# Performance work log

Hardware: AMD Instinct MI355X
Metric: run time of the kernel (lower is better)

## Reference

```python
import jax, jax.numpy as jnp
import numpy as np

B, S_EN, S_FR, EMB, UNITS, V_EN, V_FR = 64, 64, 64, 512, 1024, 32000, 16000


def setup_inputs() -> dict:
    key = jax.random.key(0)
    ks = jax.random.split(key, 16)
    sc = 0.05
    inp = {
        "en": jax.random.randint(ks[0], (B, S_EN), 0, V_EN, dtype=jnp.int32),
        "fr": jax.random.randint(ks[1], (B, S_FR), 0, V_FR, dtype=jnp.int32),
        "valid_len": jax.random.randint(ks[2], (B,), 1, S_EN, dtype=jnp.int32),
        "en_emb": jax.random.normal(ks[3], (V_EN, EMB), jnp.float32) * sc,
        "de_emb": jax.random.normal(ks[4], (V_FR, EMB), jnp.float32) * sc,
        "en_W": jax.random.normal(ks[5], (EMB, 4 * UNITS), jnp.float32) * sc,
        "en_U": jax.random.normal(ks[6], (UNITS, 4 * UNITS), jnp.float32) * sc,
        "en_b": jnp.zeros((4 * UNITS,), jnp.float32),
        "de_W": jax.random.normal(ks[7], (UNITS + EMB, 4 * UNITS), jnp.float32) * sc,
        "de_U": jax.random.normal(ks[8], (UNITS, 4 * UNITS), jnp.float32) * sc,
        "de_b": jnp.zeros((4 * UNITS,), jnp.float32),
        "Wq": jax.random.normal(ks[9], (UNITS, UNITS), jnp.float32) * sc,
        "Wk": jax.random.normal(ks[10], (UNITS, UNITS), jnp.float32) * sc,
        "wv": jax.random.normal(ks[11], (UNITS, 1), jnp.float32) * sc,
        "Wd": jax.random.normal(ks[12], (UNITS, V_FR), jnp.float32) * sc,
        "bd": jnp.zeros((V_FR,), jnp.float32),
    }
    return inp


def _lstm_step(h, c, x, W, Uw, b):
    # keras gate order: i, f, g(candidate), o
    z = x @ W + h @ Uw + b
    i, f, g, o = jnp.split(z, 4, axis=-1)
    c = jax.nn.sigmoid(f) * c + jax.nn.sigmoid(i) * jnp.tanh(g)
    h = jax.nn.sigmoid(o) * jnp.tanh(c)
    return h, c


def reference(en, fr, valid_len, en_emb, de_emb, en_W, en_U, en_b,
              de_W, de_U, de_b, Wq, Wk, wv, Wd, bd):
    b = en.shape[0]
    u = en_U.shape[0]
    # ----- Encode -----
    x_en = en_emb[en]                       # (B, S_en, E)
    h0 = jnp.zeros((b, u), x_en.dtype)

    def enc_step(carry, xt):
        h, c = carry
        h, c = _lstm_step(h, c, xt, en_W, en_U, en_b)
        return (h, c), h

    (h, c), en_o = jax.lax.scan(enc_step, (h0, h0), jnp.swapaxes(x_en, 0, 1))
    en_o = jnp.swapaxes(en_o, 0, 1)         # (B, S_en, U)

    # ----- Decode with additive attention per step -----
    kproj = en_o @ Wk                       # (B, S_en, U), key proj is step-invariant
    pos = jnp.arange(en.shape[1])
    attn_mask = pos[None, :] < valid_len[:, None]   # (B, S_en)
    x_fr = de_emb[fr]                       # (B, S_fr, E)

    def dec_step(carry, xt):
        h, c = carry
        q = h @ Wq                          # (B, U)
        feat = jnp.tanh(q[:, None, :] + kproj)      # (B, S_en, U)
        score = jnp.squeeze(feat @ wv, -1)          # (B, S_en)
        score = jnp.where(attn_mask, score, -1000000.0)
        attn = jax.nn.softmax(score, axis=-1)
        context = jnp.einsum('bs,bsu->bu', attn, en_o)
        x = jnp.concatenate([context, xt], axis=-1)  # (B, U+E)
        h, c = _lstm_step(h, c, x, de_W, de_U, de_b)
        return (h, c), h

    (_, _), hs = jax.lax.scan(dec_step, (h, c), jnp.swapaxes(x_fr, 0, 1))
    logits = jnp.swapaxes(hs, 0, 1) @ Wd + bd       # (B, S_fr, V_fr)
    return logits
```

## Files before the change

### kernel.cpp

```cpp
#include <hip/hip_runtime.h>
#include <math.h>

#define BD    64
#define SEQ   64
#define EMBD  512
#define UNITS 1024
#define NG    4096
#define VFR   16000

typedef __attribute__((ext_vector_type(8))) short bf16x8;
typedef __attribute__((ext_vector_type(4))) float f32x4;

__device__ __forceinline__ float sigm(float x) { return 1.0f / (1.0f + __expf(-x)); }
__device__ __forceinline__ float tanh_f(float x) {
    float e = __expf(2.0f * x);
    return 1.0f - 2.0f / (e + 1.0f);
}
__device__ __forceinline__ unsigned bf16bits(float v) {
    unsigned u = __float_as_uint(v);
    return (u + 0x7FFFu + ((u >> 16) & 1u)) >> 16;
}
__device__ __forceinline__ float bf2f(short s) {
    return __uint_as_float(((unsigned)(unsigned short)s) << 16);
}
__device__ __forceinline__ void split2(float v, short& h, short& l) {
    unsigned hb = bf16bits(v);
    float hv = __uint_as_float(hb << 16);
    h = (short)hb;
    l = (short)bf16bits(v - hv);
}

__device__ __forceinline__ void gbar(int* cnt, int* gen, int nb) {
    __threadfence();
    __syncthreads();
    if (threadIdx.x == 0) {
        int g = __hip_atomic_load(gen, __ATOMIC_RELAXED, __HIP_MEMORY_SCOPE_AGENT);
        if (atomicAdd(cnt, 1) == nb - 1) {
            __hip_atomic_store(cnt, 0, __ATOMIC_RELAXED, __HIP_MEMORY_SCOPE_AGENT);
            __hip_atomic_store(gen, g + 1, __ATOMIC_RELEASE, __HIP_MEMORY_SCOPE_AGENT);
        } else {
            while (__hip_atomic_load(gen, __ATOMIC_RELAXED, __HIP_MEMORY_SCOPE_AGENT) == g)
                __builtin_amdgcn_s_sleep(8);
        }
    }
    __syncthreads();
    __threadfence();
}

__global__ __launch_bounds__(64) void zero16(int* p) {
    if (threadIdx.x < 16) p[threadIdx.x] = 0;
}

__global__ __launch_bounds__(256) void gather_bf16(
    const float* __restrict__ emb, const int* __restrict__ idx,
    short* __restrict__ dst, int K)
{
    int row = blockIdx.x;
    int g = idx[row];
    const float* src = emb + (size_t)g * K;
    for (int k = threadIdx.x * 2; k < K; k += 512) {
        float2 v = *(const float2*)&src[k];
        dst[(size_t)row * K + k]     = (short)bf16bits(v.x);
        dst[(size_t)row * K + k + 1] = (short)bf16bits(v.y);
    }
}

template <bool SPLIT>
__global__ __launch_bounds__(256) void transp_split(
    const float* __restrict__ src, int N, int K,
    short* __restrict__ dh, short* __restrict__ dl)
{
    __shared__ float sm[32][33];
    const int tid = threadIdx.x;
    const int nt = blockIdx.x * 32, kt = blockIdx.y * 32;
    {
        int r = tid >> 3, c4 = (tid & 7) * 4;
        float4 v = *(const float4*)&src[(size_t)(kt + r) * N + nt + c4];
        sm[r][c4] = v.x; sm[r][c4 + 1] = v.y; sm[r][c4 + 2] = v.z; sm[r][c4 + 3] = v.w;
    }
    __syncthreads();
    {
        int n = tid >> 3, k4 = (tid & 7) * 4;
        short4 hh, ll;
        short a, b;
        split2(sm[k4 + 0][n], a, b); hh.x = a; ll.x = b;
        split2(sm[k4 + 1][n], a, b); hh.y = a; ll.y = b;
        split2(sm[k4 + 2][n], a, b); hh.z = a; ll.z = b;
        split2(sm[k4 + 3][n], a, b); hh.w = a; ll.w = b;
        *(short4*)&dh[(size_t)(nt + n) * K + kt + k4] = hh;
        if (SPLIT) *(short4*)&dl[(size_t)(nt + n) * K + kt + k4] = ll;
    }
}

template <int OMODE, bool SA, bool SB>
__global__ __launch_bounds__(256, 2) void gemm_split(
    const short* __restrict__ Ah, const short* __restrict__ Al,
    const short* __restrict__ Bh, const short* __restrict__ Bl,
    const float* __restrict__ bias, void* __restrict__ Cout, int N, int K)
{
    __shared__ short lds[32 * 512];
    const int tid = threadIdx.x;
    const int lane = tid & 63, w = tid >> 6;
    const int bm = blockIdx.y, bn = blockIdx.x;
    const int wm = w & 1, wn = w >> 1;
    const int r15 = lane & 15, q = lane >> 4;

    f32x4 zero4 = {0.f, 0.f, 0.f, 0.f};
    f32x4 acc[4][4];
#pragma unroll
    for (int i = 0; i < 4; ++i)
#pragma unroll
        for (int j = 0; j < 4; ++j) acc[i][j] = zero4;

    const short* gsrc[8];
    bool use[8];
#pragma unroll
    for (int i = 0; i < 8; ++i) {
        int st = w * 8 + i;
        int mat = st >> 4, hl = (st >> 3) & 1, mt = st & 7;
        const short* base = (mat == 0) ? (hl ? Al : Ah) : (hl ? Bl : Bh);
        use[i] = (mat == 0) ? (SA || hl == 0) : (SB || hl == 0);
        int row = ((mat == 0) ? bm : bn) * 128 + mt * 16 + r15;
        gsrc[i] = base + (size_t)row * K + q * 8;
    }

    for (int k0 = 0; k0 < K; k0 += 32) {
        int4 stg[8];
#pragma unroll
        for (int i = 0; i < 8; ++i)
            if (use[i]) stg[i] = *(const int4*)(gsrc[i] + k0);
        __syncthreads();
#pragma unroll
        for (int i = 0; i < 8; ++i)
            if (use[i]) *(int4*)&lds[(size_t)((w * 8 + i) * 64 + lane) * 8] = stg[i];
        __syncthreads();

        bf16x8 ah[4], al[4], bh[4], bl[4];
#pragma unroll
        for (int i = 0; i < 4; ++i) {
            ah[i] = *(const bf16x8*)&lds[(((wm * 4 + i) * 64) + lane) * 8];
            if (SA) al[i] = *(const bf16x8*)&lds[(((8 + wm * 4 + i) * 64) + lane) * 8];
            bh[i] = *(const bf16x8*)&lds[(((16 + wn * 4 + i) * 64) + lane) * 8];
            if (SB) bl[i] = *(const bf16x8*)&lds[(((24 + wn * 4 + i) * 64) + lane) * 8];
        }
#pragma unroll
        for (int i = 0; i < 4; ++i)
#pragma unroll
            for (int j = 0; j < 4; ++j) {
                acc[i][j] = __builtin_amdgcn_mfma_f32_16x16x32_bf16(ah[i], bh[j], acc[i][j], 0, 0, 0);
                if (SA) acc[i][j] = __builtin_amdgcn_mfma_f32_16x16x32_bf16(al[i], bh[j], acc[i][j], 0, 0, 0);
                if (SB) acc[i][j] = __builtin_amdgcn_mfma_f32_16x16x32_bf16(ah[i], bl[j], acc[i][j], 0, 0, 0);
            }
    }

#pragma unroll
    for (int i = 0; i < 4; ++i) {
        int rowbase = bm * 128 + wm * 64 + i * 16 + q * 4;
#pragma unroll
        for (int j = 0; j < 4; ++j) {
            int col = bn * 128 + wn * 64 + j * 16 + r15;
            float bv = bias ? bias[col] : 0.f;
#pragma unroll
            for (int rI = 0; rI < 4; ++rI) {
                int row = rowbase + rI;
                float v = acc[i][j][rI] + bv;
                if (OMODE == 1) {
                    int orow = ((row & 63) << 6) | (row >> 6);
                    ((float*)Cout)[(size_t)orow * N + col] = v;
                } else if (OMODE == 0) {
                    ((float*)Cout)[(size_t)row * N + col] = v;
                } else {
                    ((short*)Cout)[(size_t)row * N + col] = (short)bf16bits(v);
                }
            }
        }
    }
}

__device__ __forceinline__ void accum_hU(
    float& a0, float& a1, const float* __restrict__ h_ws,
    const float* __restrict__ U, int n, int b0, int tid,
    float (*hsm)[66])
{
    for (int k0 = 0; k0 < 1024; k0 += 64) {
        __syncthreads();
#pragma unroll
        for (int i = 0; i < 2; ++i) {
            int idx4 = tid * 2 + i;
            int bb = idx4 >> 4, kq = (idx4 & 15) * 4;
            float4 v = *(const float4*)&h_ws[bb * 1024 + k0 + kq];
            hsm[kq + 0][bb] = v.x;
            hsm[kq + 1][bb] = v.y;
            hsm[kq + 2][bb] = v.z;
            hsm[kq + 3][bb] = v.w;
        }
        __syncthreads();
#pragma unroll 8
        for (int kk = 0; kk < 64; ++kk) {
            float uv = U[(size_t)(k0 + kk) * NG + n];
            float2 hv = *(const float2*)&hsm[kk][b0];
            a0 += hv.x * uv;
            a1 += hv.y * uv;
        }
    }
}

__device__ __forceinline__ void lstm_gate_phase(
    int t, int blk, int tid, const float* __restrict__ z_ws,
    float* __restrict__ h_ws, float* __restrict__ c_ws,
    short* __restrict__ oh, short* __restrict__ ol)
{
    int g2 = blk * 512 + tid;
    if (g2 < 65536) {
        int b = g2 >> 10, u = g2 & 1023;
        const float* zr = z_ws + b * NG;
        float zi = zr[u], zf = zr[u + 1024], zg = zr[u + 2048], zo = zr[u + 3072];
        float cp = c_ws[g2];
        float cn = sigm(zf) * cp + sigm(zi) * tanh_f(zg);
        float hn = sigm(zo) * tanh_f(cn);
        c_ws[g2] = cn;
        h_ws[g2] = hn;
        short hh, hl;
        split2(hn, hh, hl);
        size_t o = (size_t)(t * 64 + b) * 1024 + u;
        oh[o] = hh;
        ol[o] = hl;
    }
}

__global__ __launch_bounds__(512, 2) void encoder_persist(
    const short* __restrict__ xW,
    const float* __restrict__ U,
    float* __restrict__ h_ws, float* __restrict__ c_ws, float* __restrict__ z_ws,
    short* __restrict__ eo_h, short* __restrict__ eo_l,
    int* cnt, int* gen)
{
    __shared__ float hsm[64][66];
    const int tid = threadIdx.x;
    const int blk = blockIdx.x;
    {
        int g = blk * 512 + tid;
        if (g < 65536) h_ws[g] = 0.f;
        else c_ws[g - 65536] = 0.f;
    }
    gbar(cnt, gen, 256);
    const int c16 = tid & 15, bg = tid >> 4;
    const int n = blk * 16 + c16;
    const int b0 = bg * 2;
    for (int t = 0; t < SEQ; ++t) {
        float a0 = bf2f(xW[(size_t)(b0 * 64 + t) * NG + n]);
        float a1 = bf2f(xW[(size_t)((b0 + 1) * 64 + t) * NG + n]);
        accum_hU(a0, a1, h_ws, U, n, b0, tid, hsm);
        z_ws[b0 * NG + n] = a0;
        z_ws[(b0 + 1) * NG + n] = a1;
        gbar(cnt, gen, 256);
        lstm_gate_phase(t, blk, tid, z_ws, h_ws, c_ws, eo_h, eo_l);
        gbar(cnt, gen, 256);
    }
}

__global__ __launch_bounds__(512, 2) void decoder_persist(
    const short* __restrict__ xW,
    const float* __restrict__ U,
    const float* __restrict__ Wq, const float* __restrict__ wv,
    const float* __restrict__ kproj,
    const float* __restrict__ EOWc,
    const int* __restrict__ valid_len,
    float* __restrict__ h_ws, float* __restrict__ c_ws, float* __restrict__ z_ws,
    float* __restrict__ q_ws, float* __restrict__ sc_ws,
    short* __restrict__ hs_h, short* __restrict__ hs_l,
    int* cnt, int* gen)
{
    __shared__ float hsm[64][66];
    __shared__ float attn_sm[64][65];
    __shared__ float redq[64][8][4];
    const int tid = threadIdx.x;
    const int blk = blockIdx.x;

    for (int t = 0; t < SEQ; ++t) {
        {
            const int b = tid & 63;
            const int p8 = tid >> 6;
            const int kbase = p8 * 128;
            const int u0 = blk * 4;
            float ax = 0.f, ay = 0.f, az = 0.f, aw = 0.f;
            const float* hrow = h_ws + b * 1024 + kbase;
            const float* wbase = Wq + (size_t)kbase * 1024 + u0;
#pragma unroll 8
            for (int k = 0; k < 128; k += 4) {
                float4 hv = *(const float4*)&hrow[k];
                float4 w0 = *(const float4*)&wbase[(size_t)(k + 0) * 1024];
                float4 w1 = *(const float4*)&wbase[(size_t)(k + 1) * 1024];
                float4 w2 = *(const float4*)&wbase[(size_t)(k + 2) * 1024];
                float4 w3 = *(const float4*)&wbase[(size_t)(k + 3) * 1024];
                ax += hv.x * w0.x + hv.y * w1.x + hv.z * w2.x + hv.w * w3.x;
                ay += hv.x * w0.y + hv.y * w1.y + hv.z * w2.y + hv.w * w3.y;
                az += hv.x * w0.z + hv.y * w1.z + hv.z * w2.z + hv.w * w3.z;
                aw += hv.x * w0.w + hv.y * w1.w + hv.z * w2.w + hv.w * w3.w;
            }
            redq[b][p8][0] = ax; redq[b][p8][1] = ay;
            redq[b][p8][2] = az; redq[b][p8][3] = aw;
            __syncthreads();
            if (tid < 64) {
                float sx = 0.f, sy = 0.f, sz = 0.f, sw = 0.f;
#pragma unroll
                for (int p = 0; p < 8; ++p) {
                    sx += redq[tid][p][0]; sy += redq[tid][p][1];
                    sz += redq[tid][p][2]; sw += redq[tid][p][3];
                }
                float4 o = {sx, sy, sz, sw};
                *(float4*)&q_ws[tid * 1024 + u0] = o;
            }
        }
        gbar(cnt, gen, 256);
        {
            const int p = tid >> 5, l32 = tid & 31;
            const int pair = blk * 16 + p;
            const int b = pair & 63, s = pair >> 6;
            const float* kp = kproj + (size_t)pair * 1024;
            const float* qp = q_ws + b * 1024;
            float a = 0.f;
#pragma unroll
            for (int j = 0; j < 8; ++j) {
                int k = j * 128 + l32 * 4;
                float4 kv = *(const float4*)&kp[k];
                float4 qv = *(const float4*)&qp[k];
                float4 w4 = *(const float4*)&wv[k];
                a += w4.x * tanh_f(qv.x + kv.x);
                a += w4.y * tanh_f(qv.y + kv.y);
                a += w4.z * tanh_f(qv.z + kv.z);
                a += w4.w * tanh_f(qv.w + kv.w);
            }
#pragma unroll
            for (int off = 16; off; off >>= 1) a += __shfl_xor(a, off, 64);
            if (l32 == 0) sc_ws[b * 64 + s] = a;
        }
        gbar(cnt, gen, 256);
        {
            if (tid < 64) {
                const int b = tid;
                const int vl = valid_len[b];
                float mx = -1e30f;
                for (int s = 0; s < 64; ++s) {
                    float v = (s < vl) ? sc_ws[b * 64 + s] : -1000000.0f;
                    attn_sm[b][s] = v;
                    mx = fmaxf(mx, v);
                }
                float sum = 0.f;
                for (int s = 0; s < 64; ++s) {
                    float e = __expf(attn_sm[b][s] - mx);
                    attn_sm[b][s] = e;
                    sum += e;
                }
                float r = 1.f / sum;
                for (int s = 0; s < 64; ++s) attn_sm[b][s] *= r;
            }
            __syncthreads();
            const int c16 = tid & 15, bg = tid >> 4;
            const int n = blk * 16 + c16;
            const int b0 = bg * 2;
            float a0 = bf2f(xW[(size_t)(b0 * 64 + t) * NG + n]);
            float a1 = bf2f(xW[(size_t)((b0 + 1) * 64 + t) * NG + n]);
#pragma unroll 4
            for (int s = 0; s < 64; ++s) {
                float w0 = attn_sm[b0][s], w1 = attn_sm[b0 + 1][s];
                a0 += w0 * EOWc[(size_t)(s * 64 + b0) * NG + n];
                a1 += w1 * EOWc[(size_t)(s * 64 + b0 + 1) * NG + n];
            }
            accum_hU(a0, a1, h_ws, U, n, b0, tid, hsm);
            z_ws[b0 * NG + n] = a0;
            z_ws[(b0 + 1) * NG + n] = a1;
        }
        gbar(cnt, gen, 256);
        lstm_gate_phase(t, blk, tid, z_ws, h_ws, c_ws, hs_h, hs_l);
        gbar(cnt, gen, 256);
    }
}

extern "C" void kernel_launch(void* const* d_in, const int* in_sizes, int n_in,
                              void* d_out, int out_size, void* d_ws, size_t ws_size,
                              hipStream_t stream)
{
    const int*   en        = (const int*)d_in[0];
    const int*   fr        = (const int*)d_in[1];
    const int*   valid_len = (const int*)d_in[2];
    const float* en_emb    = (const float*)d_in[3];
    const float* de_emb    = (const float*)d_in[4];
    const float* en_W      = (const float*)d_in[5];
    const float* en_U      = (const float*)d_in[6];
    const float* en_b      = (const float*)d_in[7];
    const float* de_W      = (const float*)d_in[8];
    const float* de_U      = (const float*)d_in[9];
    const float* de_b      = (const float*)d_in[10];
    const float* Wq        = (const float*)d_in[11];
    const float* Wk        = (const float*)d_in[12];
    const float* wv        = (const float*)d_in[13];
    const float* Wd        = (const float*)d_in[14];
    const float* bd        = (const float*)d_in[15];
    float* out = (float*)d_out;
    char*  ws  = (char*)d_ws;

    float* EOWC  = (float*)(ws + 0);
    short* WDT_H = (short*)(ws + 0);
    short* WDT_L = (short*)(ws + 33554432);
    short* XWEN  = (short*)(ws + 67108864);
    float* KPROJ = (float*)(ws + 67108864);
    short* XWFR  = (short*)(ws + 100663296);
    short* XEN   = (short*)(ws + 134217728);
    short* XFR   = (short*)(ws + 138412032);
    short* WCT_H = (short*)(ws + 134217728);
    short* WCT_L = (short*)(ws + 142606336);
    short* HS_H  = (short*)(ws + 134217728);
    short* HS_L  = (short*)(ws + 142606336);
    short* ENWT  = (short*)(ws + 150994944);
    short* WXT   = (short*)(ws + 155189248);
    short* EO_H  = (short*)(ws + 150994944);
    short* EO_L  = (short*)(ws + 159383552);
    short* WKT_H = (short*)(ws + 167772160);
    short* WKT_L = (short*)(ws + 169869312);
    float* ZWS   = (float*)(ws + 171966464);
    float* HWS   = (float*)(ws + 173015040);
    float* CWS   = (float*)(ws + 173277184);
    float* QWS   = (float*)(ws + 173539328);
    float* SCWS  = (float*)(ws + 173801472);
    int*   BAR   = (int*)(ws + 173817856);

    zero16<<<1, 64, 0, stream>>>(BAR);

    gather_bf16<<<4096, 256, 0, stream>>>(en_emb, en, XEN, EMBD);
    gather_bf16<<<4096, 256, 0, stream>>>(de_emb, fr, XFR, EMBD);
    transp_split<false><<<dim3(128, 16), 256, 0, stream>>>(en_W, NG, EMBD, ENWT, nullptr);
    transp_split<false><<<dim3(128, 16), 256, 0, stream>>>(de_W + (size_t)UNITS * NG, NG, EMBD, WXT, nullptr);

    gemm_split<2, false, false><<<dim3(32, 32), 256, 0, stream>>>(
        XEN, XEN, ENWT, ENWT, en_b, XWEN, NG, EMBD);
    gemm_split<2, false, false><<<dim3(32, 32), 256, 0, stream>>>(
        XFR, XFR, WXT, WXT, de_b, XWFR, NG, EMBD);

    transp_split<true><<<dim3(128, 32), 256, 0, stream>>>(de_W, NG, UNITS, WCT_H, WCT_L);

    encoder_persist<<<256, 512, 0, stream>>>(XWEN, en_U, HWS, CWS, ZWS, EO_H, EO_L, BAR, BAR + 8);

    gemm_split<0, true, true><<<dim3(32, 32), 256, 0, stream>>>(
        EO_H, EO_L, WCT_H, WCT_L, nullptr, EOWC, NG, UNITS);

    transp_split<true><<<dim3(32, 32), 256, 0, stream>>>(Wk, UNITS, UNITS, WKT_H, WKT_L);
    gemm_split<0, true, true><<<dim3(8, 32), 256, 0, stream>>>(
        EO_H, EO_L, WKT_H, WKT_L, nullptr, KPROJ, UNITS, UNITS);

    decoder_persist<<<256, 512, 0, stream>>>(
        XWFR, de_U, Wq, wv, KPROJ, EOWC, valid_len,
        HWS, CWS, ZWS, QWS, SCWS, HS_H, HS_L, BAR, BAR + 8);

    transp_split<true><<<dim3(500, 32), 256, 0, stream>>>(Wd, VFR, UNITS, WDT_H, WDT_L);
    gemm_split<1, true, true><<<dim3(125, 32), 256, 0, stream>>>(
        HS_H, HS_L, WDT_H, WDT_L, bd, out, VFR, UNITS);
}
```

Before: 42.00 ms.

## Transpose recurrent weights and encoder-context product for contiguous vectorized loads

Adds an fp32 transpose kernel and pre-transposes the encoder and decoder recurrent weight matrices, so each thread reads its weight column as contiguous float4 vectors held in registers. The encoder-output times context-weight GEMM now writes in a layout where the sequence axis is innermost, so the decoder's attention-weighted context sum becomes contiguous float4 loads. The attention LDS row is padded to 68 floats to keep float4 reads aligned. This removes strided scalar global loads in the latency-bound recurrent loops, at the cost of extra transpose passes, more workspace, and higher register pressure.

```diff
diff --git a/kernel.cpp b/kernel.cpp
--- a/kernel.cpp
+++ b/kernel.cpp
@@ -92,6 +92,27 @@
     }
 }
 
+__global__ __launch_bounds__(256) void transp_f32(
+    const float* __restrict__ src, int N, int K, float* __restrict__ dst)
+{
+    __shared__ float sm[32][33];
+    const int tid = threadIdx.x;
+    const int nt = blockIdx.x * 32, kt = blockIdx.y * 32;
+    {
+        int r = tid >> 3, c4 = (tid & 7) * 4;
+        float4 v = *(const float4*)&src[(size_t)(kt + r) * N + nt + c4];
+        sm[r][c4] = v.x; sm[r][c4 + 1] = v.y; sm[r][c4 + 2] = v.z; sm[r][c4 + 3] = v.w;
+    }
+    __syncthreads();
+    {
+        int n = tid >> 3, k4 = (tid & 7) * 4;
+        float4 o;
+        o.x = sm[k4 + 0][n]; o.y = sm[k4 + 1][n];
+        o.z = sm[k4 + 2][n]; o.w = sm[k4 + 3][n];
+        *(float4*)&dst[(size_t)(nt + n) * K + kt + k4] = o;
+    }
+}
+
 template <int OMODE, bool SA, bool SB>
 __global__ __launch_bounds__(256, 2) void gemm_split(
     const short* __restrict__ Ah, const short* __restrict__ Al,
@@ -169,6 +190,8 @@
                     ((float*)Cout)[(size_t)orow * N + col] = v;
                 } else if (OMODE == 0) {
                     ((float*)Cout)[(size_t)row * N + col] = v;
+                } else if (OMODE == 3) {
+                    ((float*)Cout)[((size_t)(row & 63) * N + col) * 64 + (row >> 6)] = v;
                 } else {
                     ((short*)Cout)[(size_t)row * N + col] = (short)bf16bits(v);
                 }
@@ -177,12 +200,16 @@
     }
 }
 
-__device__ __forceinline__ void accum_hU(
+__device__ __forceinline__ void accum_hUT(
     float& a0, float& a1, const float* __restrict__ h_ws,
-    const float* __restrict__ U, int n, int b0, int tid,
+    const float* __restrict__ UT, int n, int b0, int tid,
     float (*hsm)[66])
 {
+    const float4* ut = (const float4*)&UT[(size_t)n * 1024];
     for (int k0 = 0; k0 < 1024; k0 += 64) {
+        float4 uvr[16];
+#pragma unroll
+        for (int i = 0; i < 16; ++i) uvr[i] = ut[(k0 >> 2) + i];
         __syncthreads();
 #pragma unroll
         for (int i = 0; i < 2; ++i) {
@@ -195,12 +222,15 @@
             hsm[kq + 3][bb] = v.w;
         }
         __syncthreads();
-#pragma unroll 8
-        for (int kk = 0; kk < 64; ++kk) {
-            float uv = U[(size_t)(k0 + kk) * NG + n];
-            float2 hv = *(const float2*)&hsm[kk][b0];
-            a0 += hv.x * uv;
-            a1 += hv.y * uv;
+#pragma unroll
+        for (int kk4 = 0; kk4 < 16; ++kk4) {
+            float4 uv = uvr[kk4];
+            float2 h0v = *(const float2*)&hsm[kk4 * 4 + 0][b0];
+            float2 h1v = *(const float2*)&hsm[kk4 * 4 + 1][b0];
+            float2 h2v = *(const float2*)&hsm[kk4 * 4 + 2][b0];
+            float2 h3v = *(const float2*)&hsm[kk4 * 4 + 3][b0];
+            a0 += h0v.x * uv.x + h1v.x * uv.y + h2v.x * uv.z + h3v.x * uv.w;
+            a1 += h0v.y * uv.x + h1v.y * uv.y + h2v.y * uv.z + h3v.y * uv.w;
         }
     }
 }
@@ -230,7 +260,7 @@
 
 __global__ __launch_bounds__(512, 2) void encoder_persist(
     const short* __restrict__ xW,
-    const float* __restrict__ U,
+    const float* __restrict__ UT,
     float* __restrict__ h_ws, float* __restrict__ c_ws, float* __restrict__ z_ws,
     short* __restrict__ eo_h, short* __restrict__ eo_l,
     int* cnt, int* gen)
@@ -250,7 +280,7 @@
     for (int t = 0; t < SEQ; ++t) {
         float a0 = bf2f(xW[(size_t)(b0 * 64 + t) * NG + n]);
         float a1 = bf2f(xW[(size_t)((b0 + 1) * 64 + t) * NG + n]);
-        accum_hU(a0, a1, h_ws, U, n, b0, tid, hsm);
+        accum_hUT(a0, a1, h_ws, UT, n, b0, tid, hsm);
         z_ws[b0 * NG + n] = a0;
         z_ws[(b0 + 1) * NG + n] = a1;
         gbar(cnt, gen, 256);
@@ -261,10 +291,10 @@
 
 __global__ __launch_bounds__(512, 2) void decoder_persist(
     const short* __restrict__ xW,
-    const float* __restrict__ U,
+    const float* __restrict__ UT,
     const float* __restrict__ Wq, const float* __restrict__ wv,
     const float* __restrict__ kproj,
-    const float* __restrict__ EOWc,
+    const float* __restrict__ EOT,
     const int* __restrict__ valid_len,
     float* __restrict__ h_ws, float* __restrict__ c_ws, float* __restrict__ z_ws,
     float* __restrict__ q_ws, float* __restrict__ sc_ws,
@@ -272,7 +302,7 @@
     int* cnt, int* gen)
 {
     __shared__ float hsm[64][66];
-    __shared__ float attn_sm[64][65];
+    __shared__ float attn_sm[64][68];
     __shared__ float redq[64][8][4];
     const int tid = threadIdx.x;
     const int blk = blockIdx.x;
@@ -361,13 +391,18 @@
             const int b0 = bg * 2;
             float a0 = bf2f(xW[(size_t)(b0 * 64 + t) * NG + n]);
             float a1 = bf2f(xW[(size_t)((b0 + 1) * 64 + t) * NG + n]);
-#pragma unroll 4
-            for (int s = 0; s < 64; ++s) {
-                float w0 = attn_sm[b0][s], w1 = attn_sm[b0 + 1][s];
-                a0 += w0 * EOWc[(size_t)(s * 64 + b0) * NG + n];
-                a1 += w1 * EOWc[(size_t)(s * 64 + b0 + 1) * NG + n];
-            }
-            accum_hU(a0, a1, h_ws, U, n, b0, tid, hsm);
+            const float4* e0 = (const float4*)&EOT[((size_t)b0 * 4096 + n) * 64];
+            const float4* e1 = e0 + 65536;
+            const float4* w0p = (const float4*)&attn_sm[b0][0];
+            const float4* w1p = (const float4*)&attn_sm[b0 + 1][0];
+#pragma unroll
+            for (int s4 = 0; s4 < 16; ++s4) {
+                float4 v0 = e0[s4], v1 = e1[s4];
+                float4 x0 = w0p[s4], x1 = w1p[s4];
+                a0 += v0.x * x0.x + v0.y * x0.y + v0.z * x0.z + v0.w * x0.w;
+                a1 += v1.x * x1.x + v1.y * x1.y + v1.z * x1.z + v1.w * x1.w;
+            }
+            accum_hUT(a0, a1, h_ws, UT, n, b0, tid, hsm);
             z_ws[b0 * NG + n] = a0;
             z_ws[(b0 + 1) * NG + n] = a1;
         }
@@ -400,11 +435,13 @@
     float* out = (float*)d_out;
     char*  ws  = (char*)d_ws;
 
-    float* EOWC  = (float*)(ws + 0);
+    float* ENUT  = (float*)(ws + 0);
+    float* EOT   = (float*)(ws + 0);
     short* WDT_H = (short*)(ws + 0);
     short* WDT_L = (short*)(ws + 33554432);
     short* XWEN  = (short*)(ws + 67108864);
     float* KPROJ = (float*)(ws + 67108864);
+    float* DEUT  = (float*)(ws + 83886080);
     short* XWFR  = (short*)(ws + 100663296);
     short* XEN   = (short*)(ws + 134217728);
     short* XFR   = (short*)(ws + 138412032);
@@ -431,6 +468,7 @@
     gather_bf16<<<4096, 256, 0, stream>>>(de_emb, fr, XFR, EMBD);
     transp_split<false><<<dim3(128, 16), 256, 0, stream>>>(en_W, NG, EMBD, ENWT, nullptr);
     transp_split<false><<<dim3(128, 16), 256, 0, stream>>>(de_W + (size_t)UNITS * NG, NG, EMBD, WXT, nullptr);
+    transp_f32<<<dim3(128, 32), 256, 0, stream>>>(en_U, NG, UNITS, ENUT);
 
     gemm_split<2, false, false><<<dim3(32, 32), 256, 0, stream>>>(
         XEN, XEN, ENWT, ENWT, en_b, XWEN, NG, EMBD);
@@ -439,17 +477,19 @@
 
     transp_split<true><<<dim3(128, 32), 256, 0, stream>>>(de_W, NG, UNITS, WCT_H, WCT_L);
 
-    encoder_persist<<<256, 512, 0, stream>>>(XWEN, en_U, HWS, CWS, ZWS, EO_H, EO_L, BAR, BAR + 8);
-
-    gemm_split<0, true, true><<<dim3(32, 32), 256, 0, stream>>>(
-        EO_H, EO_L, WCT_H, WCT_L, nullptr, EOWC, NG, UNITS);
+    encoder_persist<<<256, 512, 0, stream>>>(XWEN, ENUT, HWS, CWS, ZWS, EO_H, EO_L, BAR, BAR + 8);
+
+    transp_f32<<<dim3(128, 32), 256, 0, stream>>>(de_U, NG, UNITS, DEUT);
+
+    gemm_split<3, true, true><<<dim3(32, 32), 256, 0, stream>>>(
+        EO_H, EO_L, WCT_H, WCT_L, nullptr, EOT, NG, UNITS);
 
     transp_split<true><<<dim3(32, 32), 256, 0, stream>>>(Wk, UNITS, UNITS, WKT_H, WKT_L);
     gemm_split<0, true, true><<<dim3(8, 32), 256, 0, stream>>>(
         EO_H, EO_L, WKT_H, WKT_L, nullptr, KPROJ, UNITS, UNITS);
 
     decoder_persist<<<256, 512, 0, stream>>>(
-        XWFR, de_U, Wq, wv, KPROJ, EOWC, valid_len,
+        XWFR, DEUT, Wq, wv, KPROJ, EOT, valid_len,
         HWS, CWS, ZWS, QWS, SCWS, HS_H, HS_L, BAR, BAR + 8);
 
     transp_split<true><<<dim3(500, 32), 256, 0, stream>>>(Wd, VFR, UNITS, WDT_H, WDT_L);
```

Result: slower. 46.82 ms (+11.5%).
